# Performance work log

Measured on AMD Instinct MI355X. Metric: run time of the kernel, lower is better.

Reference implementation:

```python
import jax, jax.numpy as jnp
import numpy as np

# init kwargs (constants)
P = 1            # chamfer_distance_p
WEIGHT = 1.0
XYZ_UNIT = 0.1


def setup_inputs() -> dict:
    key = jax.random.key(0)
    k1, k2 = jax.random.split(key)
    B, N, M, D = 16, 4096, 4096, 3
    pred = jax.random.normal(k1, (B, N, D), dtype=jnp.float32)
    gt = jax.random.normal(k2, (B, M, D), dtype=jnp.float32)
    return {"pred": pred, "gt": gt}


def _chamfer(x, y, p):
    x2 = jnp.sum(x * x, axis=-1)                       # [B, N]
    y2 = jnp.sum(y * y, axis=-1)                       # [B, M]
    xy = jnp.einsum('bnd,bmd->bnm', x, y)              # [B, N, M]
    sq = jnp.maximum(x2[:, :, None] + y2[:, None, :] - 2.0 * xy, 0.0)
    dist = jnp.sqrt(sq)                                # torch.norm(x-y, dim=3)
    if p != 1:
        dist = dist ** p
    x_loss = jnp.mean(jnp.min(dist, axis=2), axis=1)   # [B]
    y_loss = jnp.mean(jnp.min(dist, axis=1), axis=1)   # [B]
    return jnp.mean(x_loss + y_loss)                   # scalar (reduce=True)


def reference(pred, gt):
    # HelperPointLoss.forward with reduce_over_batch=True, loss_name='chamfer_distance'
    loss = _chamfer(pred, gt, P)
    # info['helper_loss'] = loss (detached); info['helper_cderr'] = p=1 chamfer * xyz_unit
    cderr = _chamfer(pred, gt, 1) * XYZ_UNIT
    return (WEIGHT * loss, loss, cderr)
```

## Files before the change

kernel.cpp:

```cpp
#include <hip/hip_runtime.h>
#include <hip/hip_fp16.h>

typedef __attribute__((ext_vector_type(8)))  _Float16 half8;
typedef __attribute__((ext_vector_type(16))) float    f32x16;

#define B_   16
#define NPTS 4096

constexpr int BLK  = 256;
constexpr int WV   = 4;
constexpr int QPW  = 32;
constexpr int QPB  = WV * QPW;
constexpr int NQC  = NPTS / QPB;
constexpr int RT   = 1024;
constexpr int NR   = NPTS / RT;
constexpr int TPR  = RT / 32;
constexpr int NBLK = 2 * B_ * NQC;

__device__ __forceinline__ float min3f(float a, float b, float c) {
    return fminf(fminf(a, b), c);
}

__global__ __launch_bounds__(BLK, 4) void chamfer_mfma(
        const float* __restrict__ pred, const float* __restrict__ gt,
        float* __restrict__ accum, unsigned* __restrict__ counter,
        float* __restrict__ out) {
    const int qc  = blockIdx.x;
    const int b   = blockIdx.y;
    const int dir = blockIdx.z;
    const float* qsrc = dir ? gt   : pred;
    const float* tsrc = dir ? pred : gt;

    __shared__ uint4 sh[RT];
    __shared__ float ps[WV];

    const int tid  = threadIdx.x;
    const int lane = tid & 63;
    const int wv   = tid >> 6;
    const int m    = lane & 31;

    const float* qp = qsrc + (b * NPTS + qc * QPB + wv * QPW + m) * 3;
    __half hqx = __float2half(qp[0]);
    __half hqy = __float2half(qp[1]);
    __half hqz = __float2half(qp[2]);
    float fqx = __half2float(hqx), fqy = __half2float(hqy), fqz = __half2float(hqz);
    const float q2 = fmaf(fqx, fqx, fmaf(fqy, fqy, fqz * fqz));
    uint4 bu;
    bu.x = (unsigned)__half_as_ushort(hqx) | ((unsigned)__half_as_ushort(hqy) << 16);
    bu.y = (unsigned)__half_as_ushort(hqz) | (0x3C00u << 16);
    bu.z = 0x3C00u;
    bu.w = 0u;
    const half8 bfrag = __builtin_bit_cast(half8, bu);

    f32x16 zero;
#pragma unroll
    for (int i = 0; i < 16; ++i) zero[i] = 0.0f;
    f32x16 mn;
#pragma unroll
    for (int i = 0; i < 16; ++i) mn[i] = 1e30f;

    for (int r = 0; r < NR; ++r) {
        if (r) __syncthreads();
        const float* tp = tsrc + (b * NPTS + r * RT) * 3;
#pragma unroll
        for (int k = 0; k < RT / BLK; ++k) {
            int j = k * BLK + tid;
            __half hx = __float2half(tp[3 * j + 0]);
            __half hy = __float2half(tp[3 * j + 1]);
            __half hz = __float2half(tp[3 * j + 2]);
            float fx = __half2float(hx), fy = __half2float(hy), fz = __half2float(hz);
            float g2 = fmaf(fx, fx, fmaf(fy, fy, fz * fz));
            __half ax = __float2half(-2.0f * fx);
            __half ay = __float2half(-2.0f * fy);
            __half az = __float2half(-2.0f * fz);
            __half g2hi = __float2half(g2);
            __half g2lo = __float2half(g2 - __half2float(g2hi));
            uint4 w;
            w.x = (unsigned)__half_as_ushort(ax) | ((unsigned)__half_as_ushort(ay) << 16);
            w.y = (unsigned)__half_as_ushort(az) | ((unsigned)__half_as_ushort(g2hi) << 16);
            w.z = (unsigned)__half_as_ushort(g2lo);
            w.w = 0u;
            sh[j] = w;
        }
        __syncthreads();

#pragma unroll 4
        for (int t = 0; t < TPR; t += 2) {
            uint4 au0 = sh[t * 32 + m];
            uint4 au1 = sh[t * 32 + 32 + m];
            half8 a0 = __builtin_bit_cast(half8, au0);
            half8 a1 = __builtin_bit_cast(half8, au1);
            f32x16 d0 = __builtin_amdgcn_mfma_f32_32x32x16_f16(a0, bfrag, zero, 0, 0, 0);
            f32x16 d1 = __builtin_amdgcn_mfma_f32_32x32x16_f16(a1, bfrag, zero, 0, 0, 0);
#pragma unroll
            for (int i = 0; i < 16; ++i)
                mn[i] = min3f(mn[i], d0[i], d1[i]);
        }
    }

    float a0 = min3f(mn[0],  mn[1],  mn[2]);
    float a1 = min3f(mn[3],  mn[4],  mn[5]);
    float a2 = min3f(mn[6],  mn[7],  mn[8]);
    float a3 = min3f(mn[9],  mn[10], mn[11]);
    float a4 = min3f(mn[12], mn[13], mn[14]);
    float v  = fminf(min3f(a0, a1, a2), min3f(a3, a4, mn[15]));
    v = fminf(v, __shfl_xor(v, 32));

    float dd = fmaxf(fmaf(0.5f, v, q2), 0.0f);
    float s  = sqrtf(dd);
#pragma unroll
    for (int off = 32; off; off >>= 1) s += __shfl_xor(s, off);
    if (lane == 0) ps[wv] = 0.5f * s;
    __syncthreads();

    if (tid == 0) {
        atomicAdd(accum, ps[0] + ps[1] + ps[2] + ps[3]);
        __threadfence();
        if (atomicAdd(counter, 1u) == NBLK - 1) {
            float total = atomicAdd(accum, 0.0f);
            float loss  = total * (1.0f / (float)(B_ * NPTS));
            out[0] = loss;
            out[1] = loss;
            out[2] = 0.1f * loss;
        }
    }
}

extern "C" void kernel_launch(void* const* d_in, const int* in_sizes, int n_in,
                              void* d_out, int out_size, void* d_ws, size_t ws_size,
                              hipStream_t stream) {
    const float* pred = (const float*)d_in[0];
    const float* gt   = (const float*)d_in[1];
    float*    out     = (float*)d_out;
    float*    accum   = (float*)d_ws;
    unsigned* counter = (unsigned*)d_ws + 1;

    hipMemsetAsync(d_ws, 0, 8, stream);
    chamfer_mfma<<<dim3(NQC, B_, 2), BLK, 0, stream>>>(pred, gt, accum, counter, out);
}
```

Before: 91.91 us.

## Precompute packed fp16 target rows in a prep kernel and stream them from global memory

Adds a prep kernel that converts every target point once into the packed fp16 A-fragment format (scaled coordinates plus split squared norm) in workspace. The main kernel then reads these rows straight from global memory instead of having every block reconvert all targets into LDS behind barriers. The B fragment is split into lower and upper K halves so each wave covers 64 distinct targets per pair of MFMAs, which removes the doubled norm term and the 0.5 correction. The trade is an extra kernel launch and extra global/L2 traffic in the inner loop, with no shared-memory staging.

```diff
diff --git a/kernel.cpp b/kernel.cpp
--- a/kernel.cpp
+++ b/kernel.cpp
@@ -7,31 +7,53 @@
 #define B_   16
 #define NPTS 4096
 
-constexpr int BLK  = 256;
-constexpr int WV   = 4;
-constexpr int QPW  = 32;
-constexpr int QPB  = WV * QPW;
-constexpr int NQC  = NPTS / QPB;
-constexpr int RT   = 1024;
-constexpr int NR   = NPTS / RT;
-constexpr int TPR  = RT / 32;
-constexpr int NBLK = 2 * B_ * NQC;
+constexpr int BLK   = 256;
+constexpr int WV    = 4;
+constexpr int QPW   = 32;
+constexpr int QPB   = WV * QPW;
+constexpr int NQC   = NPTS / QPB;
+constexpr int NIT   = NPTS / 64;
+constexpr int NBLK  = 2 * B_ * NQC;
+constexpr int HALF  = B_ * NPTS;
 
 __device__ __forceinline__ float min3f(float a, float b, float c) {
     return fminf(fminf(a, b), c);
 }
 
-__global__ __launch_bounds__(BLK, 4) void chamfer_mfma(
+__global__ void prep_kernel(const float* __restrict__ pred,
+                            const float* __restrict__ gt,
+                            uint4* __restrict__ arow) {
+    int i = blockIdx.x * blockDim.x + threadIdx.x;
+    const float* src = (i < HALF) ? gt : pred;
+    int j = (i < HALF) ? i : i - HALF;
+    __half hx = __float2half(src[3 * j + 0]);
+    __half hy = __float2half(src[3 * j + 1]);
+    __half hz = __float2half(src[3 * j + 2]);
+    float fx = __half2float(hx), fy = __half2float(hy), fz = __half2float(hz);
+    float g2 = fmaf(fx, fx, fmaf(fy, fy, fz * fz));
+    __half ax = __float2half(-2.0f * fx);
+    __half ay = __float2half(-2.0f * fy);
+    __half az = __float2half(-2.0f * fz);
+    __half g2hi = __float2half(g2);
+    __half g2lo = __float2half(g2 - __half2float(g2hi));
+    uint4 w;
+    w.x = (unsigned)__half_as_ushort(ax) | ((unsigned)__half_as_ushort(ay) << 16);
+    w.y = (unsigned)__half_as_ushort(az) | ((unsigned)__half_as_ushort(g2hi) << 16);
+    w.z = (unsigned)__half_as_ushort(g2lo);
+    w.w = 0u;
+    arow[i] = w;
+}
+
+__global__ __launch_bounds__(BLK, 4) void chamfer_main(
         const float* __restrict__ pred, const float* __restrict__ gt,
+        const uint4* __restrict__ arow,
         float* __restrict__ accum, unsigned* __restrict__ counter,
         float* __restrict__ out) {
     const int qc  = blockIdx.x;
     const int b   = blockIdx.y;
     const int dir = blockIdx.z;
-    const float* qsrc = dir ? gt   : pred;
-    const float* tsrc = dir ? pred : gt;
+    const float* qsrc = dir ? gt : pred;
 
-    __shared__ uint4 sh[RT];
     __shared__ float ps[WV];
 
     const int tid  = threadIdx.x;
@@ -50,7 +72,15 @@
     bu.y = (unsigned)__half_as_ushort(hqz) | (0x3C00u << 16);
     bu.z = 0x3C00u;
     bu.w = 0u;
-    const half8 bfrag = __builtin_bit_cast(half8, bu);
+    const uint4 zu = make_uint4(0u, 0u, 0u, 0u);
+    const bool lo = (lane < 32);
+    uint4 bLu, bHu;
+    bLu.x = lo ? bu.x : 0u; bLu.y = lo ? bu.y : 0u;
+    bLu.z = lo ? bu.z : 0u; bLu.w = 0u;
+    bHu.x = lo ? 0u : bu.x; bHu.y = lo ? 0u : bu.y;
+    bHu.z = lo ? 0u : bu.z; bHu.w = 0u;
+    const half8 bL = __builtin_bit_cast(half8, bLu);
+    const half8 bH = __builtin_bit_cast(half8, bHu);
 
     f32x16 zero;
 #pragma unroll
@@ -59,43 +89,16 @@
 #pragma unroll
     for (int i = 0; i < 16; ++i) mn[i] = 1e30f;
 
-    for (int r = 0; r < NR; ++r) {
-        if (r) __syncthreads();
-        const float* tp = tsrc + (b * NPTS + r * RT) * 3;
+    const uint4* ap = arow + dir * HALF + b * NPTS + lane;
+#pragma unroll 4
+    for (int it = 0; it < NIT; ++it) {
+        uint4 au = ap[it * 64];
+        half8 a = __builtin_bit_cast(half8, au);
+        f32x16 d0 = __builtin_amdgcn_mfma_f32_32x32x16_f16(a, bL, zero, 0, 0, 0);
+        f32x16 d1 = __builtin_amdgcn_mfma_f32_32x32x16_f16(a, bH, zero, 0, 0, 0);
 #pragma unroll
-        for (int k = 0; k < RT / BLK; ++k) {
-            int j = k * BLK + tid;
-            __half hx = __float2half(tp[3 * j + 0]);
-            __half hy = __float2half(tp[3 * j + 1]);
-            __half hz = __float2half(tp[3 * j + 2]);
-            float fx = __half2float(hx), fy = __half2float(hy), fz = __half2float(hz);
-            float g2 = fmaf(fx, fx, fmaf(fy, fy, fz * fz));
-            __half ax = __float2half(-2.0f * fx);
-            __half ay = __float2half(-2.0f * fy);
-            __half az = __float2half(-2.0f * fz);
-            __half g2hi = __float2half(g2);
-            __half g2lo = __float2half(g2 - __half2float(g2hi));
-            uint4 w;
-            w.x = (unsigned)__half_as_ushort(ax) | ((unsigned)__half_as_ushort(ay) << 16);
-            w.y = (unsigned)__half_as_ushort(az) | ((unsigned)__half_as_ushort(g2hi) << 16);
-            w.z = (unsigned)__half_as_ushort(g2lo);
-            w.w = 0u;
-            sh[j] = w;
-        }
-        __syncthreads();
-
-#pragma unroll 4
-        for (int t = 0; t < TPR; t += 2) {
-            uint4 au0 = sh[t * 32 + m];
-            uint4 au1 = sh[t * 32 + 32 + m];
-            half8 a0 = __builtin_bit_cast(half8, au0);
-            half8 a1 = __builtin_bit_cast(half8, au1);
-            f32x16 d0 = __builtin_amdgcn_mfma_f32_32x32x16_f16(a0, bfrag, zero, 0, 0, 0);
-            f32x16 d1 = __builtin_amdgcn_mfma_f32_32x32x16_f16(a1, bfrag, zero, 0, 0, 0);
-#pragma unroll
-            for (int i = 0; i < 16; ++i)
-                mn[i] = min3f(mn[i], d0[i], d1[i]);
-        }
+        for (int i = 0; i < 16; ++i)
+            mn[i] = min3f(mn[i], d0[i], d1[i]);
     }
 
     float a0 = min3f(mn[0],  mn[1],  mn[2]);
@@ -106,7 +109,7 @@
     float v  = fminf(min3f(a0, a1, a2), min3f(a3, a4, mn[15]));
     v = fminf(v, __shfl_xor(v, 32));
 
-    float dd = fmaxf(fmaf(0.5f, v, q2), 0.0f);
+    float dd = fmaxf(v + q2, 0.0f);
     float s  = sqrtf(dd);
 #pragma unroll
     for (int off = 32; off; off >>= 1) s += __shfl_xor(s, off);
@@ -131,10 +134,14 @@
                               hipStream_t stream) {
     const float* pred = (const float*)d_in[0];
     const float* gt   = (const float*)d_in[1];
-    float*    out     = (float*)d_out;
+    float* out = (float*)d_out;
+
     float*    accum   = (float*)d_ws;
     unsigned* counter = (unsigned*)d_ws + 1;
+    uint4*    arow    = (uint4*)((char*)d_ws + 1024);
 
     hipMemsetAsync(d_ws, 0, 8, stream);
-    chamfer_mfma<<<dim3(NQC, B_, 2), BLK, 0, stream>>>(pred, gt, accum, counter, out);
+    prep_kernel<<<dim3(2 * HALF / 256), 256, 0, stream>>>(pred, gt, arow);
+    chamfer_main<<<dim3(NQC, B_, 2), BLK, 0, stream>>>(pred, gt, arow,
+                                                       accum, counter, out);
 }
```

Result: slower. 97.32 us (+5.9%).
